# Optimization experiments

Hardware: AMD Instinct MI355X
Metric: run time of the kernel (lower is better)

## Reference

```python
import jax, jax.numpy as jnp
import numpy as np

WINDOW_SIZE = 11
SIGMA = 1.5
C_IN = 3

def _gaussian_window():
    coords = jnp.arange(WINDOW_SIZE, dtype=jnp.float32) - WINDOW_SIZE // 2
    g = jnp.exp(-(coords ** 2) / (2.0 * SIGMA ** 2))
    g = g / g.sum()
    win = g[:, None] * g[None, :]                       # [11, 11]
    return jnp.broadcast_to(win[None, None], (C_IN, 1, WINDOW_SIZE, WINDOW_SIZE))

def _depthwise_conv(x, w):
    pad = WINDOW_SIZE // 2
    return jax.lax.conv_general_dilated(
        x, w,
        window_strides=(1, 1),
        padding=[(pad, pad), (pad, pad)],
        dimension_numbers=('NCHW', 'OIHW', 'NCHW'),
        feature_group_count=C_IN)

def setup_inputs() -> dict:
    key = jax.random.key(0)
    k1, k2 = jax.random.split(key)
    clean = jax.random.uniform(k1, (32, 3, 512, 512), dtype=jnp.float32)
    adversarial = jax.random.uniform(k2, (32, 3, 512, 512), dtype=jnp.float32)
    return {"clean": clean, "adversarial": adversarial}

def reference(clean, adversarial):
    C1 = 0.01 ** 2
    C2 = 0.03 ** 2
    w = _gaussian_window()
    mu1 = _depthwise_conv(clean, w)
    mu2 = _depthwise_conv(adversarial, w)
    mu1_sq = mu1 ** 2
    mu2_sq = mu2 ** 2
    mu12 = mu1 * mu2
    sigma1_sq = _depthwise_conv(clean ** 2, w) - mu1_sq
    sigma2_sq = _depthwise_conv(adversarial ** 2, w) - mu2_sq
    sigma12 = _depthwise_conv(clean * adversarial, w) - mu12
    ssim_map = ((2.0 * mu12 + C1) * (2.0 * sigma12 + C2)) / (
        (mu1_sq + mu2_sq + C1) * (sigma1_sq + sigma2_sq + C2))
    return 1.0 - ssim_map.mean()
```

## Files before the change

kernel.cpp:

```cpp
#include <hip/hip_runtime.h>


typedef float v2f __attribute__((ext_vector_type(2)));
typedef float v4f __attribute__((ext_vector_type(4)));

#define IMG 512
#define TILE 64
#define HALO 5
#define LROWS 74
#define LCOLS 74
#define LSTRIDE 76
#define LSTRIDE4 38
#define RPT 4
#define NPIX 25165824.0

__device__ constexpr float WT[11] = {
    0.00102838f, 0.00759876f, 0.03600077f, 0.10936068f, 0.21300552f,
    0.26601173f,
    0.21300552f, 0.10936068f, 0.03600077f, 0.00759876f, 0.00102838f};

__global__ __launch_bounds__(512)
__attribute__((amdgpu_waves_per_eu(6, 6)))
void ssim_main(const float* __restrict__ clean,
               const float* __restrict__ adv,
               double* __restrict__ accum)
{
    __shared__ __align__(16) v2f tile[LROWS * LSTRIDE];
    __shared__ float wpart[8];

    const int tid = threadIdx.x;
    const int b = blockIdx.x;
    const int plane = b >> 6;
    const int t6 = b & 63;
    const int tile_x = (t6 & 7) * TILE;
    const int tile_y = (t6 >> 3) * TILE;

    const float* __restrict__ cp = clean + (size_t)plane * (IMG * IMG);
    const float* __restrict__ ap = adv   + (size_t)plane * (IMG * IMG);

    for (int idx = tid; idx < LROWS * LCOLS; idx += 512) {
        int r = idx / LCOLS;
        int c = idx - r * LCOLS;
        int gr = tile_y + r - HALO;
        int gc = tile_x + c - HALO;
        v2f v = {0.f, 0.f};
        if (gr >= 0 && gr < IMG && gc >= 0 && gc < IMG) {
            int gi = gr * IMG + gc;
            float x = cp[gi];
            float y = ap[gi];
            v.x = x + y;
            v.y = x - y;
        }
        tile[r * LSTRIDE + c] = v;
    }
    __syncthreads();

    const int cpair = tid & 31;
    const int strip = tid >> 5;
    const int r0 = strip * RPT;
    const v4f* __restrict__ tile4 = (const v4f*)tile;

    v2f aA0[RPT], aA1[RPT], aB0[RPT], aB1[RPT];
    #pragma unroll
    for (int o = 0; o < RPT; ++o) {
        aA0[o] = (v2f){0.f, 0.f}; aA1[o] = (v2f){0.f, 0.f};
        aB0[o] = (v2f){0.f, 0.f}; aB1[o] = (v2f){0.f, 0.f};
    }

    #pragma unroll
    for (int j = 0; j < RPT + 10; ++j) {
        const v4f* bp = tile4 + (r0 + j) * LSTRIDE4 + cpair;
        v4f q0 = bp[0], q1 = bp[1], q2 = bp[2], q3 = bp[3], q4 = bp[4], q5 = bp[5];
        v2f t[12];
        t[0]  = (v2f){q0.x, q0.y}; t[1]  = (v2f){q0.z, q0.w};
        t[2]  = (v2f){q1.x, q1.y}; t[3]  = (v2f){q1.z, q1.w};
        t[4]  = (v2f){q2.x, q2.y}; t[5]  = (v2f){q2.z, q2.w};
        t[6]  = (v2f){q3.x, q3.y}; t[7]  = (v2f){q3.z, q3.w};
        t[8]  = (v2f){q4.x, q4.y}; t[9]  = (v2f){q4.z, q4.w};
        t[10] = (v2f){q5.x, q5.y}; t[11] = (v2f){q5.z, q5.w};

        v2f hA0 = {0.f, 0.f}, hA1 = {0.f, 0.f};
        v2f hB0 = {0.f, 0.f}, hB1 = {0.f, 0.f};
        #pragma unroll
        for (int k = 0; k < 12; ++k) {
            v2f tv = t[k];
            v2f pp = tv * tv;
            if (k < 11) {
                const float w = WT[k];
                hA0 += w * tv; hB0 += w * pp;
            }
            if (k > 0) {
                const float w = WT[k - 1];
                hA1 += w * tv; hB1 += w * pp;
            }
        }

        #pragma unroll
        for (int o = 0; o < RPT; ++o) {
            const int kv = j - o;
            if (kv >= 0 && kv < 11) {
                const float w = WT[kv];
                aA0[o] += w * hA0; aA1[o] += w * hA1;
                aB0[o] += w * hB0; aB1[o] += w * hB1;
            }
        }
    }

    const float C1 = 1e-4f;
    const float C2 = 9e-4f;
    float lsum = 0.f;
    #pragma unroll
    for (int o = 0; o < RPT; ++o) {
        #pragma unroll
        for (int s = 0; s < 2; ++s) {
            v2f a  = s ? aA1[o] : aA0[o];
            v2f bb = s ? aB1[o] : aB0[o];
            float U = a.x * a.x;
            float V = a.y * a.y;
            float halfUmV = 0.5f * (U - V);
            float halfUpV = 0.5f * (U + V);
            float num1 = halfUmV + C1;
            float num2 = 0.5f * (bb.x - bb.y) - halfUmV + C2;
            float den1 = halfUpV + C1;
            float den2 = 0.5f * (bb.x + bb.y) - halfUpV + C2;
            lsum += (num1 * num2) * __builtin_amdgcn_rcpf(den1 * den2);
        }
    }

    #pragma unroll
    for (int off = 32; off > 0; off >>= 1)
        lsum += __shfl_down(lsum, off);
    const int lane = tid & 63;
    const int wave = tid >> 6;
    if (lane == 0) wpart[wave] = lsum;
    __syncthreads();
    if (tid == 0) {
        float bs = 0.f;
        #pragma unroll
        for (int w = 0; w < 8; ++w) bs += wpart[w];
        atomicAdd(accum, (double)bs);
    }
}

__global__ void ssim_finalize(const double* __restrict__ accum,
                              float* __restrict__ out)
{
    if (threadIdx.x == 0) {
        out[0] = 1.f - (float)(accum[0] / NPIX);
    }
}

extern "C" void kernel_launch(void* const* d_in, const int* in_sizes, int n_in,
                              void* d_out, int out_size, void* d_ws, size_t ws_size,
                              hipStream_t stream)
{
    const float* clean = (const float*)d_in[0];
    const float* adv   = (const float*)d_in[1];
    float* out = (float*)d_out;
    double* accum = (double*)d_ws;

    hipMemsetAsync(accum, 0, sizeof(double), stream);

    const int nblocks = 96 * 64;
    ssim_main<<<nblocks, 512, 0, stream>>>(clean, adv, accum);
    ssim_finalize<<<1, 64, 0, stream>>>(accum, out);
}
```

Measured before the change: 314.9 us.

## Do vertical pass from global into registers, store to LDS, then horizontal pass

The separable filter is restructured: each thread now loads a column segment straight from global memory and runs the vertical 11-tap pass in registers, writing the vertical sums (A and B) into a shared buffer. A second phase then runs the horizontal pass per row from that buffer. This removes the full raw-tile LDS stage and the per-row horizontal recompute of the old layout, so LDS traffic should drop. In exchange, 592 column units over 512 threads leave the load phase unbalanced, the shared buffer doubles in size, and occupancy is lowered to 4 waves per EU.

Measured after the change: 368.3 us. 17.0% more time.

```diff
diff --git a/kernel.cpp b/kernel.cpp
--- a/kernel.cpp
+++ b/kernel.cpp
@@ -7,11 +7,10 @@
 #define IMG 512
 #define TILE 64
 #define HALO 5
-#define LROWS 74
-#define LCOLS 74
-#define LSTRIDE 76
-#define LSTRIDE4 38
-#define RPT 4
+#define HCOLS 74
+#define HSTRIDE 75
+#define SEGS 8
+#define RPT1 8
 #define NPIX 25165824.0
 
 __device__ constexpr float WT[11] = {
@@ -20,12 +19,12 @@
     0.21300552f, 0.10936068f, 0.03600077f, 0.00759876f, 0.00102838f};
 
 __global__ __launch_bounds__(512)
-__attribute__((amdgpu_waves_per_eu(6, 6)))
+__attribute__((amdgpu_waves_per_eu(4, 4)))
 void ssim_main(const float* __restrict__ clean,
                const float* __restrict__ adv,
                double* __restrict__ accum)
 {
-    __shared__ __align__(16) v2f tile[LROWS * LSTRIDE];
+    __shared__ __align__(16) v4f hbuf[TILE * HSTRIDE];
     __shared__ float wpart[8];
 
     const int tid = threadIdx.x;
@@ -38,70 +37,75 @@
     const float* __restrict__ cp = clean + (size_t)plane * (IMG * IMG);
     const float* __restrict__ ap = adv   + (size_t)plane * (IMG * IMG);
 
-    for (int idx = tid; idx < LROWS * LCOLS; idx += 512) {
-        int r = idx / LCOLS;
-        int c = idx - r * LCOLS;
-        int gr = tile_y + r - HALO;
-        int gc = tile_x + c - HALO;
-        v2f v = {0.f, 0.f};
-        if (gr >= 0 && gr < IMG && gc >= 0 && gc < IMG) {
-            int gi = gr * IMG + gc;
-            float x = cp[gi];
-            float y = ap[gi];
-            v.x = x + y;
-            v.y = x - y;
+    for (int u = tid; u < HCOLS * SEGS; u += 512) {
+        const int seg = u / HCOLS;
+        const int uc  = u - seg * HCOLS;
+        const int col = tile_x + uc - HALO;
+        const bool cvalid = ((unsigned)col < IMG);
+        const int or0 = seg * RPT1;
+
+        v2f accA[RPT1], accB[RPT1];
+        #pragma unroll
+        for (int o = 0; o < RPT1; ++o) {
+            accA[o] = (v2f){0.f, 0.f};
+            accB[o] = (v2f){0.f, 0.f};
         }
-        tile[r * LSTRIDE + c] = v;
-    }
-    __syncthreads();
 
-    const int cpair = tid & 31;
-    const int strip = tid >> 5;
-    const int r0 = strip * RPT;
-    const v4f* __restrict__ tile4 = (const v4f*)tile;
-
-    v2f aA0[RPT], aA1[RPT], aB0[RPT], aB1[RPT];
-    #pragma unroll
-    for (int o = 0; o < RPT; ++o) {
-        aA0[o] = (v2f){0.f, 0.f}; aA1[o] = (v2f){0.f, 0.f};
-        aB0[o] = (v2f){0.f, 0.f}; aB1[o] = (v2f){0.f, 0.f};
-    }
-
-    #pragma unroll
-    for (int j = 0; j < RPT + 10; ++j) {
-        const v4f* bp = tile4 + (r0 + j) * LSTRIDE4 + cpair;
-        v4f q0 = bp[0], q1 = bp[1], q2 = bp[2], q3 = bp[3], q4 = bp[4], q5 = bp[5];
-        v2f t[12];
-        t[0]  = (v2f){q0.x, q0.y}; t[1]  = (v2f){q0.z, q0.w};
-        t[2]  = (v2f){q1.x, q1.y}; t[3]  = (v2f){q1.z, q1.w};
-        t[4]  = (v2f){q2.x, q2.y}; t[5]  = (v2f){q2.z, q2.w};
-        t[6]  = (v2f){q3.x, q3.y}; t[7]  = (v2f){q3.z, q3.w};
-        t[8]  = (v2f){q4.x, q4.y}; t[9]  = (v2f){q4.z, q4.w};
-        t[10] = (v2f){q5.x, q5.y}; t[11] = (v2f){q5.z, q5.w};
-
-        v2f hA0 = {0.f, 0.f}, hA1 = {0.f, 0.f};
-        v2f hB0 = {0.f, 0.f}, hB1 = {0.f, 0.f};
         #pragma unroll
-        for (int k = 0; k < 12; ++k) {
-            v2f tv = t[k];
-            v2f pp = tv * tv;
-            if (k < 11) {
-                const float w = WT[k];
-                hA0 += w * tv; hB0 += w * pp;
+        for (int j = 0; j < RPT1 + 10; ++j) {
+            const int gr = tile_y + or0 - HALO + j;
+            v2f t = {0.f, 0.f};
+            if (cvalid && (unsigned)gr < IMG) {
+                const int gi = gr * IMG + col;
+                const float x = cp[gi];
+                const float y = ap[gi];
+                t.x = x + y;
+                t.y = x - y;
             }
-            if (k > 0) {
-                const float w = WT[k - 1];
-                hA1 += w * tv; hB1 += w * pp;
+            const v2f p = t * t;
+            #pragma unroll
+            for (int o = 0; o < RPT1; ++o) {
+                const int kv = j - o;
+                if (kv >= 0 && kv < 11) {
+                    const float w = WT[kv];
+                    accA[o] += w * t;
+                    accB[o] += w * p;
+                }
             }
         }
 
         #pragma unroll
-        for (int o = 0; o < RPT; ++o) {
-            const int kv = j - o;
-            if (kv >= 0 && kv < 11) {
-                const float w = WT[kv];
-                aA0[o] += w * hA0; aA1[o] += w * hA1;
-                aB0[o] += w * hB0; aB1[o] += w * hB1;
+        for (int o = 0; o < RPT1; ++o) {
+            hbuf[(or0 + o) * HSTRIDE + uc] =
+                (v4f){accA[o].x, accA[o].y, accB[o].x, accB[o].y};
+        }
+    }
+    __syncthreads();
+
+    const int row = tid & 63;
+    const int cs  = tid >> 6;
+    const int c0  = cs * 8;
+    const v4f* __restrict__ hrow = hbuf + row * HSTRIDE + c0;
+
+    v2f A[8], B[8];
+    #pragma unroll
+    for (int o = 0; o < 8; ++o) {
+        A[o] = (v2f){0.f, 0.f};
+        B[o] = (v2f){0.f, 0.f};
+    }
+
+    #pragma unroll
+    for (int k = 0; k < 18; ++k) {
+        const v4f h = hrow[k];
+        const v2f hA = {h.x, h.y};
+        const v2f hB = {h.z, h.w};
+        #pragma unroll
+        for (int o = 0; o < 8; ++o) {
+            const int kh = k - o;
+            if (kh >= 0 && kh < 11) {
+                const float w = WT[kh];
+                A[o] += w * hA;
+                B[o] += w * hB;
             }
         }
     }
@@ -110,21 +114,16 @@
     const float C2 = 9e-4f;
     float lsum = 0.f;
     #pragma unroll
-    for (int o = 0; o < RPT; ++o) {
-        #pragma unroll
-        for (int s = 0; s < 2; ++s) {
-            v2f a  = s ? aA1[o] : aA0[o];
-            v2f bb = s ? aB1[o] : aB0[o];
-            float U = a.x * a.x;
-            float V = a.y * a.y;
-            float halfUmV = 0.5f * (U - V);
-            float halfUpV = 0.5f * (U + V);
-            float num1 = halfUmV + C1;
-            float num2 = 0.5f * (bb.x - bb.y) - halfUmV + C2;
-            float den1 = halfUpV + C1;
-            float den2 = 0.5f * (bb.x + bb.y) - halfUpV + C2;
-            lsum += (num1 * num2) * __builtin_amdgcn_rcpf(den1 * den2);
-        }
+    for (int o = 0; o < 8; ++o) {
+        const float U = A[o].x * A[o].x;
+        const float V = A[o].y * A[o].y;
+        const float halfUmV = 0.5f * (U - V);
+        const float halfUpV = 0.5f * (U + V);
+        const float num1 = halfUmV + C1;
+        const float num2 = 0.5f * (B[o].x - B[o].y) - halfUmV + C2;
+        const float den1 = halfUpV + C1;
+        const float den2 = 0.5f * (B[o].x + B[o].y) - halfUpV + C2;
+        lsum += (num1 * num2) * __builtin_amdgcn_rcpf(den1 * den2);
     }
 
     #pragma unroll
```
